# Kernel tuning notes

Hardware: AMD Instinct MI355X
Metric: run time of the kernel (lower is better)

## Reference

```python
import jax, jax.numpy as jnp
import numpy as np

N = 50000      # nodes
E = 800000     # edges (avg degree 16)
D = 3          # dim_world
L = 128        # latent_dim
STEPS = 10     # message passing steps
RID = 64       # num_rigid_ids
REMB = 16      # rigid_embedding_dim


def _mlp2(x, w1, b1, w2, b2):
    # 2-layer MLP: Linear -> ReLU -> Linear (layer_norm=False, dropout=0)
    return jnp.maximum(x @ w1 + b1, 0.0) @ w2 + b2


def setup_inputs() -> dict:
    key = jax.random.key(0)
    ks = jax.random.split(key, 24)
    f32 = jnp.float32

    def lin(k, i, o):
        return (jax.random.normal(k, (i, o), f32) / np.sqrt(i)).astype(f32)

    node_in = 2 * D + 1 + REMB   # 23
    edge_in = 2 * D + 2 + 1      # 9

    receivers = jax.random.randint(ks[4], (E,), 0, N)
    # no self edges (radius_graph uses include_self_edges=False)
    senders = (receivers + jax.random.randint(ks[3], (E,), 1, N)) % N

    inp = {
        'positions': jax.random.uniform(ks[0], (N, D), f32),
        'velocities': jax.random.normal(ks[1], (N, D), f32),
        'rigid_id': jax.random.randint(ks[2], (N,), 0, RID),
        'senders': senders,
        'receivers': receivers,
        'rigid_emb': jax.random.normal(ks[5], (RID, REMB), f32) * 0.1,
        # node encoder
        'ne_w1': lin(ks[6], node_in, L), 'ne_b1': jnp.zeros((L,), f32),
        'ne_w2': lin(ks[7], L, L),       'ne_b2': jnp.zeros((L,), f32),
        # edge encoder
        'ee_w1': lin(ks[8], edge_in, L), 'ee_b1': jnp.zeros((L,), f32),
        'ee_w2': lin(ks[9], L, L),       'ee_b2': jnp.zeros((L,), f32),
        # processor blocks (stacked over STEPS)
        'pe_w1': (jax.random.normal(ks[10], (STEPS, 3 * L, L), f32) / np.sqrt(3 * L)).astype(f32),
        'pe_b1': jnp.zeros((STEPS, L), f32),
        'pe_w2': (jax.random.normal(ks[11], (STEPS, L, L), f32) / np.sqrt(L)).astype(f32),
        'pe_b2': jnp.zeros((STEPS, L), f32),
        'pn_w1': (jax.random.normal(ks[12], (STEPS, 2 * L, L), f32) / np.sqrt(2 * L)).astype(f32),
        'pn_b1': jnp.zeros((STEPS, L), f32),
        'pn_w2': (jax.random.normal(ks[13], (STEPS, L, L), f32) / np.sqrt(L)).astype(f32),
        'pn_b2': jnp.zeros((STEPS, L), f32),
        # decoder (2 layers -> output_dim = D)
        'de_w1': lin(ks[14], L, L), 'de_b1': jnp.zeros((L,), f32),
        'de_w2': lin(ks[15], L, D), 'de_b2': jnp.zeros((D,), f32),
    }
    return inp


def reference(positions, velocities, rigid_id, senders, receivers, rigid_emb,
              ne_w1, ne_b1, ne_w2, ne_b2, ee_w1, ee_b1, ee_w2, ee_b2,
              pe_w1, pe_b1, pe_w2, pe_b2, pn_w1, pn_b1, pn_w2, pn_b2,
              de_w1, de_b1, de_w2, de_b2):
    n = positions.shape[0]
    dt = positions.dtype

    # ----- feature construction (build_gns_graph_inputs + rigid features) -----
    deg = jax.ops.segment_sum(jnp.ones(receivers.shape, dt), receivers, num_segments=n)[:, None]
    center = positions.mean(axis=0, keepdims=True)
    rigid_feat = rigid_emb[rigid_id]                                # [N, REMB]
    node_feat = jnp.concatenate([velocities, positions - center, deg, rigid_feat], axis=-1)

    rel_pos = positions[senders] - positions[receivers]             # [E, D]
    rel_vel = velocities[senders] - velocities[receivers]
    sq = jnp.sum(rel_pos * rel_pos, axis=-1, keepdims=True)
    dist = jnp.sqrt(sq)
    same = (rigid_id[senders] == rigid_id[receivers]).astype(dt)[:, None]
    edge_feat = jnp.concatenate([rel_pos, rel_vel, dist, sq, same], axis=-1)

    # ----- encode -----
    nl = _mlp2(node_feat, ne_w1, ne_b1, ne_w2, ne_b2)               # [N, L]
    el = _mlp2(edge_feat, ee_w1, ee_b1, ee_w2, ee_b2)               # [E, L]

    # ----- process: gather -> edge MLP -> scatter-add -> node MLP, residual -----
    for i in range(pe_w1.shape[0]):
        edge_in = jnp.concatenate([el, nl[senders], nl[receivers]], axis=-1)  # [E, 3L]
        el = el + _mlp2(edge_in, pe_w1[i], pe_b1[i], pe_w2[i], pe_b2[i])
        agg = jax.ops.segment_sum(el, receivers, num_segments=n)              # [N, L]
        node_in = jnp.concatenate([nl, agg], axis=-1)                         # [N, 2L]
        nl = nl + _mlp2(node_in, pn_w1[i], pn_b1[i], pn_w2[i], pn_b2[i])

    # ----- decode -----
    return _mlp2(nl, de_w1, de_b1, de_w2, de_b2)                    # [N, D]
```

## Files before the change

kernel.cpp:

```cpp
#include <hip/hip_runtime.h>
#include <hip/hip_bf16.h>

#define NN 50000
#define NE 800000
#define LDIM 128
#define NSTEPS 10

typedef __hip_bfloat16 bf16;
typedef __bf16 bf8v __attribute__((ext_vector_type(8)));
typedef float f4v __attribute__((ext_vector_type(4)));
typedef unsigned short u16x8 __attribute__((ext_vector_type(8)));

__device__ inline float bflo(unsigned int u) {
    union { unsigned int i; float f; } x; x.i = u << 16; return x.f;
}
__device__ inline float bfhi(unsigned int u) {
    union { unsigned int i; float f; } x; x.i = u & 0xffff0000u; return x.f;
}
__device__ inline unsigned short f2bf(float f) {
    __hip_bfloat16 h = __float2bfloat16(f);
    unsigned short u; __builtin_memcpy(&u, &h, 2); return u;
}


__global__ void k_hist(const int* __restrict__ rcv, int* __restrict__ cnt) {
    int i = blockIdx.x * 256 + threadIdx.x;
    if (i < NE) atomicAdd(&cnt[rcv[i]], 1);
}

__global__ __launch_bounds__(1024) void k_scan(
    const int* __restrict__ cnt, int* __restrict__ row_start,
    int* __restrict__ cur, float* __restrict__ degf) {
    __shared__ int part[1024];
    const int t = threadIdx.x;
    const int CH = (NN + 1023) / 1024;
    int b0 = t * CH, b1 = b0 + CH; if (b1 > NN) b1 = NN; if (b0 > NN) b0 = NN;
    int s = 0;
    for (int i = b0; i < b1; i++) s += cnt[i];
    part[t] = s;
    __syncthreads();
    for (int off = 1; off < 1024; off <<= 1) {
        int v = (t >= off) ? part[t - off] : 0;
        __syncthreads();
        part[t] += v;
        __syncthreads();
    }
    int run = part[t] - s;
    for (int i = b0; i < b1; i++) {
        row_start[i] = run; cur[i] = run; degf[i] = (float)cnt[i];
        run += cnt[i];
    }
    if (t == 1023) row_start[NN] = part[1023];
}

__global__ void k_scatter(const int* __restrict__ snd, const int* __restrict__ rcv,
                          int* __restrict__ cur,
                          unsigned short* __restrict__ snd_p, unsigned short* __restrict__ rcv_p) {
    int i = blockIdx.x * 256 + threadIdx.x;
    if (i < NE) {
        int r = rcv[i];
        int p = atomicAdd(&cur[r], 1);
        snd_p[p] = (unsigned short)snd[i];
        rcv_p[p] = (unsigned short)r;
    }
}

__global__ void k_center(const float* __restrict__ pos, float* __restrict__ csum) {
    __shared__ float s[3][256];
    float a = 0.f, b = 0.f, c = 0.f;
    for (int i = blockIdx.x * 256 + threadIdx.x; i < NN; i += gridDim.x * 256) {
        a += pos[3 * i]; b += pos[3 * i + 1]; c += pos[3 * i + 2];
    }
    int t = threadIdx.x;
    s[0][t] = a; s[1][t] = b; s[2][t] = c;
    __syncthreads();
    for (int off = 128; off > 0; off >>= 1) {
        if (t < off) {
            s[0][t] += s[0][t + off];
            s[1][t] += s[1][t + off];
            s[2][t] += s[2][t + off];
        }
        __syncthreads();
    }
    if (t == 0) {
        atomicAdd(&csum[0], s[0][0]);
        atomicAdd(&csum[1], s[1][0]);
        atomicAdd(&csum[2], s[2][0]);
    }
}


__global__ void k_prep_w(const float* __restrict__ w, unsigned short* __restrict__ wf,
                         int KT, int Ksrc, int lo) {
    int b = blockIdx.x;
    int s = b / (KT * 8), rem = b % (KT * 8);
    int kt = rem / 8, nt = rem % 8;
    int lane = threadIdx.x, col = lane & 15, quad = lane >> 4;
    const float* W = w + (size_t)s * Ksrc * 128;
    u16x8 o;
#pragma unroll
    for (int jj = 0; jj < 8; jj++) {
        int k = kt * 32 + quad * 8 + jj;
        float x = (k < Ksrc) ? W[(size_t)k * 128 + nt * 16 + col] : 0.f;
        unsigned short h = f2bf(x);
        if (lo) h = f2bf(x - bflo(h));
        o[jj] = h;
    }
    *(u16x8*)(wf + (((size_t)b) * 64 + lane) * 8) = o;
}


__global__ __launch_bounds__(256) void k_agg(
    const unsigned short* __restrict__ el, const int* __restrict__ row_start,
    unsigned short* __restrict__ agg) {
    const int wave = threadIdx.x >> 6, lane = threadIdx.x & 63;
    const int n = blockIdx.x * 4 + wave;
    if (n >= NN) return;
    const int sub = lane >> 4, c16 = lane & 15;
    const int st = row_start[n], en = row_start[n + 1];
    float s[8];
#pragma unroll
    for (int k = 0; k < 8; k++) s[k] = 0.f;
    for (int q = st + sub; q < en; q += 4) {
        uint4 v = *(const uint4*)(el + (size_t)q * 128 + c16 * 8);
        s[0] += bflo(v.x); s[1] += bfhi(v.x);
        s[2] += bflo(v.y); s[3] += bfhi(v.y);
        s[4] += bflo(v.z); s[5] += bfhi(v.z);
        s[6] += bflo(v.w); s[7] += bfhi(v.w);
    }
#pragma unroll
    for (int k = 0; k < 8; k++) {
        s[k] += __shfl_xor(s[k], 16);
        s[k] += __shfl_xor(s[k], 32);
    }
    if (sub == 0) {
        u16x8 o;
#pragma unroll
        for (int k = 0; k < 8; k++) o[k] = f2bf(s[k]);
        *(u16x8*)(agg + (size_t)n * 128 + c16 * 8) = o;
    }
}


__global__ __launch_bounds__(256) void k_node_enc_m(
    const float* __restrict__ pos, const float* __restrict__ vel,
    const int* __restrict__ rid, const float* __restrict__ remb,
    const float* __restrict__ degf, const float* __restrict__ csum,
    const unsigned short* __restrict__ w1h, const unsigned short* __restrict__ w1l,
    const float* __restrict__ b1,
    const unsigned short* __restrict__ w2h, const unsigned short* __restrict__ w2l,
    const float* __restrict__ b2,
    float* __restrict__ nl) {
    __shared__ __align__(16) unsigned short feat_s[32 * 72];
    __shared__ __align__(16) unsigned short hid_s[32 * 264];
    const int tid = threadIdx.x, wave = tid >> 6, lane = tid & 63;
    const int col = lane & 15, quad = lane >> 4;
    bf8v W1H[2], W1L[2], W2H[4][2], W2L[4][2];
#pragma unroll
    for (int t = 0; t < 2; t++) {
        W1H[t] = *(const bf8v*)(w1h + ((size_t)(2 * wave + t) * 64 + lane) * 8);
        W1L[t] = *(const bf8v*)(w1l + ((size_t)(2 * wave + t) * 64 + lane) * 8);
    }
#pragma unroll
    for (int kt = 0; kt < 4; kt++)
#pragma unroll
        for (int t = 0; t < 2; t++) {
            W2H[kt][t] = *(const bf8v*)(w2h + ((size_t)(kt * 8 + 2 * wave + t) * 64 + lane) * 8);
            W2L[kt][t] = *(const bf8v*)(w2l + ((size_t)(kt * 8 + 2 * wave + t) * 64 + lane) * 8);
        }
    float bias1[2], bias2[2];
#pragma unroll
    for (int t = 0; t < 2; t++) {
        bias1[t] = b1[(2 * wave + t) * 16 + col];
        bias2[t] = b2[(2 * wave + t) * 16 + col];
    }
    float cx = csum[0] * (1.0f / NN), cy = csum[1] * (1.0f / NN), cz = csum[2] * (1.0f / NN);
    uint4 z = {0u, 0u, 0u, 0u};
    for (int s2 = tid; s2 < 288; s2 += 256) *(uint4*)(feat_s + s2 * 8) = z;

    for (int it = 0; it < 4; it++) {
        const int base = blockIdx.x * 128 + it * 32;
        if (base >= NN) break;
        __syncthreads();
        if (tid < 32) {
            int n = base + tid; if (n > NN - 1) n = NN - 1;
            float v[23];
            v[0] = vel[3 * n]; v[1] = vel[3 * n + 1]; v[2] = vel[3 * n + 2];
            v[3] = pos[3 * n] - cx; v[4] = pos[3 * n + 1] - cy; v[5] = pos[3 * n + 2] - cz;
            v[6] = degf[n];
            int rb = rid[n] * 16;
#pragma unroll
            for (int k = 0; k < 16; k++) v[7 + k] = remb[rb + k];
            unsigned short* f = feat_s + tid * 72;
#pragma unroll
            for (int k = 0; k < 23; k++) {
                unsigned short h = f2bf(v[k]);
                f[k] = h; f[32 + k] = f2bf(v[k] - bflo(h));
            }
        }
        __syncthreads();
        f4v acc[2][2];
#pragma unroll
        for (int mt = 0; mt < 2; mt++)
#pragma unroll
            for (int t = 0; t < 2; t++) acc[mt][t] = (f4v){0.f, 0.f, 0.f, 0.f};
        {
            bf8v a0h = *(const bf8v*)(feat_s + col * 72 + quad * 8);
            bf8v a1h = *(const bf8v*)(feat_s + (16 + col) * 72 + quad * 8);
            bf8v a0l = *(const bf8v*)(feat_s + col * 72 + 32 + quad * 8);
            bf8v a1l = *(const bf8v*)(feat_s + (16 + col) * 72 + 32 + quad * 8);
#pragma unroll
            for (int t = 0; t < 2; t++) {
                acc[0][t] = __builtin_amdgcn_mfma_f32_16x16x32_bf16(a0h, W1H[t], acc[0][t], 0, 0, 0);
                acc[1][t] = __builtin_amdgcn_mfma_f32_16x16x32_bf16(a1h, W1H[t], acc[1][t], 0, 0, 0);
                acc[0][t] = __builtin_amdgcn_mfma_f32_16x16x32_bf16(a0l, W1H[t], acc[0][t], 0, 0, 0);
                acc[1][t] = __builtin_amdgcn_mfma_f32_16x16x32_bf16(a1l, W1H[t], acc[1][t], 0, 0, 0);
                acc[0][t] = __builtin_amdgcn_mfma_f32_16x16x32_bf16(a0h, W1L[t], acc[0][t], 0, 0, 0);
                acc[1][t] = __builtin_amdgcn_mfma_f32_16x16x32_bf16(a1h, W1L[t], acc[1][t], 0, 0, 0);
            }
        }
#pragma unroll
        for (int mt = 0; mt < 2; mt++)
#pragma unroll
            for (int t = 0; t < 2; t++) {
                const int nc = (2 * wave + t) * 16 + col;
#pragma unroll
                for (int r = 0; r < 4; r++) {
                    float h = fmaxf(acc[mt][t][r] + bias1[t], 0.f);
                    unsigned short hh = f2bf(h);
                    hid_s[(mt * 16 + quad * 4 + r) * 264 + nc] = hh;
                    hid_s[(mt * 16 + quad * 4 + r) * 264 + 128 + nc] = f2bf(h - bflo(hh));
                }
            }
        __syncthreads();
#pragma unroll
        for (int mt = 0; mt < 2; mt++)
#pragma unroll
            for (int t = 0; t < 2; t++) acc[mt][t] = (f4v){0.f, 0.f, 0.f, 0.f};
#pragma unroll
        for (int kt = 0; kt < 8; kt++) {
            int w = kt & 3;
            bf8v a0 = *(const bf8v*)(hid_s + col * 264 + kt * 32 + quad * 8);
            bf8v a1 = *(const bf8v*)(hid_s + (16 + col) * 264 + kt * 32 + quad * 8);
#pragma unroll
            for (int t = 0; t < 2; t++) {
                acc[0][t] = __builtin_amdgcn_mfma_f32_16x16x32_bf16(a0, W2H[w][t], acc[0][t], 0, 0, 0);
                acc[1][t] = __builtin_amdgcn_mfma_f32_16x16x32_bf16(a1, W2H[w][t], acc[1][t], 0, 0, 0);
            }
        }
#pragma unroll
        for (int kt = 0; kt < 4; kt++) {
            bf8v a0 = *(const bf8v*)(hid_s + col * 264 + kt * 32 + quad * 8);
            bf8v a1 = *(const bf8v*)(hid_s + (16 + col) * 264 + kt * 32 + quad * 8);
#pragma unroll
            for (int t = 0; t < 2; t++) {
                acc[0][t] = __builtin_amdgcn_mfma_f32_16x16x32_bf16(a0, W2L[kt][t], acc[0][t], 0, 0, 0);
                acc[1][t] = __builtin_amdgcn_mfma_f32_16x16x32_bf16(a1, W2L[kt][t], acc[1][t], 0, 0, 0);
            }
        }
#pragma unroll
        for (int mt = 0; mt < 2; mt++)
#pragma unroll
            for (int t = 0; t < 2; t++) {
                const int nc = (2 * wave + t) * 16 + col;
#pragma unroll
                for (int r = 0; r < 4; r++) {
                    const int row = mt * 16 + quad * 4 + r;
                    if (base + row < NN)
                        nl[(size_t)(base + row) * 128 + nc] = acc[mt][t][r] + bias2[t];
                }
            }
    }
}


__global__ __launch_bounds__(256) void k_edge_enc_m(
    const float* __restrict__ pos, const float* __restrict__ vel,
    const int* __restrict__ rid,
    const unsigned short* __restrict__ snd, const unsigned short* __restrict__ rcv,
    const unsigned short* __restrict__ w1h, const unsigned short* __restrict__ w1l,
    const float* __restrict__ b1,
    const unsigned short* __restrict__ w2h, const unsigned short* __restrict__ w2l,
    const float* __restrict__ b2,
    unsigned short* __restrict__ el) {
    __shared__ __align__(16) unsigned short feat_s[32 * 72];
    __shared__ __align__(16) unsigned short hid_s[32 * 264];
    const int tid = threadIdx.x, wave = tid >> 6, lane = tid & 63;
    const int col = lane & 15, quad = lane >> 4;
    bf8v W1H[2], W1L[2], W2H[4][2], W2L[4][2];
#pragma unroll
    for (int t = 0; t < 2; t++) {
        W1H[t] = *(const bf8v*)(w1h + ((size_t)(2 * wave + t) * 64 + lane) * 8);
        W1L[t] = *(const bf8v*)(w1l + ((size_t)(2 * wave + t) * 64 + lane) * 8);
    }
#pragma unroll
    for (int kt = 0; kt < 4; kt++)
#pragma unroll
        for (int t = 0; t < 2; t++) {
            W2H[kt][t] = *(const bf8v*)(w2h + ((size_t)(kt * 8 + 2 * wave + t) * 64 + lane) * 8);
            W2L[kt][t] = *(const bf8v*)(w2l + ((size_t)(kt * 8 + 2 * wave + t) * 64 + lane) * 8);
        }
    float bias1[2], bias2[2];
#pragma unroll
    for (int t = 0; t < 2; t++) {
        bias1[t] = b1[(2 * wave + t) * 16 + col];
        bias2[t] = b2[(2 * wave + t) * 16 + col];
    }
    uint4 z = {0u, 0u, 0u, 0u};
    for (int s2 = tid; s2 < 288; s2 += 256) *(uint4*)(feat_s + s2 * 8) = z;

    for (int it = 0; it < 4; it++) {
        const int base = blockIdx.x * 128 + it * 32;
        __syncthreads();
        if (tid < 32) {
            int e = base + tid;
            int s = snd[e], r = rcv[e];
            float v[9];
            v[0] = pos[3 * s] - pos[3 * r]; v[1] = pos[3 * s + 1] - pos[3 * r + 1]; v[2] = pos[3 * s + 2] - pos[3 * r + 2];
            v[3] = vel[3 * s] - vel[3 * r]; v[4] = vel[3 * s + 1] - vel[3 * r + 1]; v[5] = vel[3 * s + 2] - vel[3 * r + 2];
            float sq = v[0] * v[0] + v[1] * v[1] + v[2] * v[2];
            v[6] = sqrtf(sq); v[7] = sq;
            v[8] = (rid[s] == rid[r]) ? 1.f : 0.f;
            unsigned short* f = feat_s + tid * 72;
#pragma unroll
            for (int k = 0; k < 9; k++) {
                unsigned short h = f2bf(v[k]);
                f[k] = h; f[32 + k] = f2bf(v[k] - bflo(h));
            }
        }
        __syncthreads();
        f4v acc[2][2];
#pragma unroll
        for (int mt = 0; mt < 2; mt++)
#pragma unroll
            for (int t = 0; t < 2; t++) acc[mt][t] = (f4v){0.f, 0.f, 0.f, 0.f};
        {
            bf8v a0h = *(const bf8v*)(feat_s + col * 72 + quad * 8);
            bf8v a1h = *(const bf8v*)(feat_s + (16 + col) * 72 + quad * 8);
            bf8v a0l = *(const bf8v*)(feat_s + col * 72 + 32 + quad * 8);
            bf8v a1l = *(const bf8v*)(feat_s + (16 + col) * 72 + 32 + quad * 8);
#pragma unroll
            for (int t = 0; t < 2; t++) {
                acc[0][t] = __builtin_amdgcn_mfma_f32_16x16x32_bf16(a0h, W1H[t], acc[0][t], 0, 0, 0);
                acc[1][t] = __builtin_amdgcn_mfma_f32_16x16x32_bf16(a1h, W1H[t], acc[1][t], 0, 0, 0);
                acc[0][t] = __builtin_amdgcn_mfma_f32_16x16x32_bf16(a0l, W1H[t], acc[0][t], 0, 0, 0);
                acc[1][t] = __builtin_amdgcn_mfma_f32_16x16x32_bf16(a1l, W1H[t], acc[1][t], 0, 0, 0);
                acc[0][t] = __builtin_amdgcn_mfma_f32_16x16x32_bf16(a0h, W1L[t], acc[0][t], 0, 0, 0);
                acc[1][t] = __builtin_amdgcn_mfma_f32_16x16x32_bf16(a1h, W1L[t], acc[1][t], 0, 0, 0);
            }
        }
#pragma unroll
        for (int mt = 0; mt < 2; mt++)
#pragma unroll
            for (int t = 0; t < 2; t++) {
                const int nc = (2 * wave + t) * 16 + col;
#pragma unroll
                for (int r = 0; r < 4; r++) {
                    float h = fmaxf(acc[mt][t][r] + bias1[t], 0.f);
                    unsigned short hh = f2bf(h);
                    hid_s[(mt * 16 + quad * 4 + r) * 264 + nc] = hh;
                    hid_s[(mt * 16 + quad * 4 + r) * 264 + 128 + nc] = f2bf(h - bflo(hh));
                }
            }
        __syncthreads();
#pragma unroll
        for (int mt = 0; mt < 2; mt++)
#pragma unroll
            for (int t = 0; t < 2; t++) acc[mt][t] = (f4v){0.f, 0.f, 0.f, 0.f};
#pragma unroll
        for (int kt = 0; kt < 8; kt++) {
            int w = kt & 3;
            bf8v a0 = *(const bf8v*)(hid_s + col * 264 + kt * 32 + quad * 8);
            bf8v a1 = *(const bf8v*)(hid_s + (16 + col) * 264 + kt * 32 + quad * 8);
#pragma unroll
            for (int t = 0; t < 2; t++) {
                acc[0][t] = __builtin_amdgcn_mfma_f32_16x16x32_bf16(a0, W2H[w][t], acc[0][t], 0, 0, 0);
                acc[1][t] = __builtin_amdgcn_mfma_f32_16x16x32_bf16(a1, W2H[w][t], acc[1][t], 0, 0, 0);
            }
        }
#pragma unroll
        for (int kt = 0; kt < 4; kt++) {
            bf8v a0 = *(const bf8v*)(hid_s + col * 264 + kt * 32 + quad * 8);
            bf8v a1 = *(const bf8v*)(hid_s + (16 + col) * 264 + kt * 32 + quad * 8);
#pragma unroll
            for (int t = 0; t < 2; t++) {
                acc[0][t] = __builtin_amdgcn_mfma_f32_16x16x32_bf16(a0, W2L[kt][t], acc[0][t], 0, 0, 0);
                acc[1][t] = __builtin_amdgcn_mfma_f32_16x16x32_bf16(a1, W2L[kt][t], acc[1][t], 0, 0, 0);
            }
        }
        __syncthreads();
#pragma unroll
        for (int mt = 0; mt < 2; mt++)
#pragma unroll
            for (int t = 0; t < 2; t++) {
                const int nc = (2 * wave + t) * 16 + col;
#pragma unroll
                for (int r = 0; r < 4; r++)
                    hid_s[(mt * 16 + quad * 4 + r) * 264 + nc] = f2bf(acc[mt][t][r] + bias2[t]);
            }
        __syncthreads();
#pragma unroll
        for (int p = 0; p < 2; p++) {
            int s2 = p * 256 + tid, e = s2 >> 4, c16 = s2 & 15;
            *(uint4*)(el + (size_t)(base + e) * 128 + c16 * 8) =
                *(const uint4*)(hid_s + e * 264 + c16 * 8);
        }
    }
}


__global__ __launch_bounds__(256) void k_edge_step(
    unsigned short* __restrict__ el, const float* __restrict__ nl,
    const unsigned short* __restrict__ snd, const unsigned short* __restrict__ rcv,
    const unsigned short* __restrict__ w1f, const float* __restrict__ b1,
    const unsigned short* __restrict__ w2f, const float* __restrict__ b2) {
    __shared__ __align__(16) unsigned short inl_s[32 * 392];
    __shared__ __align__(16) unsigned short hid_s[32 * 136];
    __shared__ int s_idx[64];
    const int tid = threadIdx.x;
    const int wave = tid >> 6, lane = tid & 63;
    const int col = lane & 15, quad = lane >> 4;

    bf8v W1[12][2], W2[4][2];
#pragma unroll
    for (int kt = 0; kt < 12; kt++)
#pragma unroll
        for (int t = 0; t < 2; t++)
            W1[kt][t] = *(const bf8v*)(w1f + ((size_t)(kt * 8 + 2 * wave + t) * 64 + lane) * 8);
#pragma unroll
    for (int kt = 0; kt < 4; kt++)
#pragma unroll
        for (int t = 0; t < 2; t++)
            W2[kt][t] = *(const bf8v*)(w2f + ((size_t)(kt * 8 + 2 * wave + t) * 64 + lane) * 8);
    float bias1[2], bias2[2];
#pragma unroll
    for (int t = 0; t < 2; t++) {
        bias1[t] = b1[(2 * wave + t) * 16 + col];
        bias2[t] = b2[(2 * wave + t) * 16 + col];
    }

    for (int it = 0; it < 4; it++) {
        const int base = blockIdx.x * 128 + it * 32;
        if (tid < 64) s_idx[tid] = (tid < 32) ? (int)snd[base + tid] : (int)rcv[base + tid - 32];
        __syncthreads();
#pragma unroll
        for (int p = 0; p < 2; p++) {
            int s = p * 256 + tid, e = s >> 4, c16 = s & 15;
            *(uint4*)(inl_s + e * 392 + c16 * 8) =
                *(const uint4*)(el + (size_t)(base + e) * 128 + c16 * 8);
            {
                const float* src = nl + (size_t)s_idx[e] * 128 + c16 * 8;
                float4 v0 = *(const float4*)src, v1 = *(const float4*)(src + 4);
                u16x8 o;
                o[0] = f2bf(v0.x); o[1] = f2bf(v0.y); o[2] = f2bf(v0.z); o[3] = f2bf(v0.w);
                o[4] = f2bf(v1.x); o[5] = f2bf(v1.y); o[6] = f2bf(v1.z); o[7] = f2bf(v1.w);
                *(u16x8*)(inl_s + e * 392 + 128 + c16 * 8) = o;
            }
            {
                const float* src = nl + (size_t)s_idx[32 + e] * 128 + c16 * 8;
                float4 v0 = *(const float4*)src, v1 = *(const float4*)(src + 4);
                u16x8 o;
                o[0] = f2bf(v0.x); o[1] = f2bf(v0.y); o[2] = f2bf(v0.z); o[3] = f2bf(v0.w);
                o[4] = f2bf(v1.x); o[5] = f2bf(v1.y); o[6] = f2bf(v1.z); o[7] = f2bf(v1.w);
                *(u16x8*)(inl_s + e * 392 + 256 + c16 * 8) = o;
            }
        }
        __syncthreads();

        f4v acc[2][2];
#pragma unroll
        for (int mt = 0; mt < 2; mt++)
#pragma unroll
            for (int t = 0; t < 2; t++) acc[mt][t] = (f4v){0.f, 0.f, 0.f, 0.f};
#pragma unroll
        for (int kt = 0; kt < 12; kt++) {
            bf8v a0 = *(const bf8v*)(inl_s + col * 392 + kt * 32 + quad * 8);
            bf8v a1 = *(const bf8v*)(inl_s + (16 + col) * 392 + kt * 32 + quad * 8);
            acc[0][0] = __builtin_amdgcn_mfma_f32_16x16x32_bf16(a0, W1[kt][0], acc[0][0], 0, 0, 0);
            acc[0][1] = __builtin_amdgcn_mfma_f32_16x16x32_bf16(a0, W1[kt][1], acc[0][1], 0, 0, 0);
            acc[1][0] = __builtin_amdgcn_mfma_f32_16x16x32_bf16(a1, W1[kt][0], acc[1][0], 0, 0, 0);
            acc[1][1] = __builtin_amdgcn_mfma_f32_16x16x32_bf16(a1, W1[kt][1], acc[1][1], 0, 0, 0);
        }
#pragma unroll
        for (int mt = 0; mt < 2; mt++)
#pragma unroll
            for (int t = 0; t < 2; t++) {
                const int nc = (2 * wave + t) * 16 + col;
#pragma unroll
                for (int r = 0; r < 4; r++) {
                    float v = fmaxf(acc[mt][t][r] + bias1[t], 0.f);
                    hid_s[(mt * 16 + quad * 4 + r) * 136 + nc] = f2bf(v);
                }
            }
        __syncthreads();

#pragma unroll
        for (int mt = 0; mt < 2; mt++)
#pragma unroll
            for (int t = 0; t < 2; t++) acc[mt][t] = (f4v){0.f, 0.f, 0.f, 0.f};
#pragma unroll
        for (int kt = 0; kt < 4; kt++) {
            bf8v a0 = *(const bf8v*)(hid_s + col * 136 + kt * 32 + quad * 8);
            bf8v a1 = *(const bf8v*)(hid_s + (16 + col) * 136 + kt * 32 + quad * 8);
            acc[0][0] = __builtin_amdgcn_mfma_f32_16x16x32_bf16(a0, W2[kt][0], acc[0][0], 0, 0, 0);
            acc[0][1] = __builtin_amdgcn_mfma_f32_16x16x32_bf16(a0, W2[kt][1], acc[0][1], 0, 0, 0);
            acc[1][0] = __builtin_amdgcn_mfma_f32_16x16x32_bf16(a1, W2[kt][0], acc[1][0], 0, 0, 0);
            acc[1][1] = __builtin_amdgcn_mfma_f32_16x16x32_bf16(a1, W2[kt][1], acc[1][1], 0, 0, 0);
        }
        __syncthreads();
#pragma unroll
        for (int mt = 0; mt < 2; mt++)
#pragma unroll
            for (int t = 0; t < 2; t++) {
                const int nc = (2 * wave + t) * 16 + col;
#pragma unroll
                for (int r = 0; r < 4; r++) {
                    const int row = mt * 16 + quad * 4 + r;
                    float v = acc[mt][t][r] + bias2[t] + bflo((unsigned int)inl_s[row * 392 + nc]);
                    hid_s[row * 136 + nc] = f2bf(v);
                }
            }
        __syncthreads();
#pragma unroll
        for (int p = 0; p < 2; p++) {
            int s = p * 256 + tid, e = s >> 4, c16 = s & 15;
            *(uint4*)(el + (size_t)(base + e) * 128 + c16 * 8) =
                *(const uint4*)(hid_s + e * 136 + c16 * 8);
        }
    }
}


__global__ __launch_bounds__(256) void k_node_step_s(
    float* __restrict__ nl, const unsigned short* __restrict__ agg,
    const unsigned short* __restrict__ w1h, const unsigned short* __restrict__ w1l,
    const float* __restrict__ b1,
    const unsigned short* __restrict__ w2h, const unsigned short* __restrict__ w2l,
    const float* __restrict__ b2) {
    __shared__ __align__(16) unsigned short a_s[32 * 392];
    __shared__ __align__(16) unsigned short hid_s[32 * 264];
    const int tid = threadIdx.x, wave = tid >> 6, lane = tid & 63;
    const int col = lane & 15, quad = lane >> 4;
    bf8v W1H[8][2], W1L[8][2], W2H[4][2], W2L[4][2];
#pragma unroll
    for (int kt = 0; kt < 8; kt++)
#pragma unroll
        for (int t = 0; t < 2; t++) {
            W1H[kt][t] = *(const bf8v*)(w1h + ((size_t)(kt * 8 + 2 * wave + t) * 64 + lane) * 8);
            W1L[kt][t] = *(const bf8v*)(w1l + ((size_t)(kt * 8 + 2 * wave + t) * 64 + lane) * 8);
        }
#pragma unroll
    for (int kt = 0; kt < 4; kt++)
#pragma unroll
        for (int t = 0; t < 2; t++) {
            W2H[kt][t] = *(const bf8v*)(w2h + ((size_t)(kt * 8 + 2 * wave + t) * 64 + lane) * 8);
            W2L[kt][t] = *(const bf8v*)(w2l + ((size_t)(kt * 8 + 2 * wave + t) * 64 + lane) * 8);
        }
    float bias1[2], bias2[2];
#pragma unroll
    for (int t = 0; t < 2; t++) {
        bias1[t] = b1[(2 * wave + t) * 16 + col];
        bias2[t] = b2[(2 * wave + t) * 16 + col];
    }
    for (int it = 0; it < 2; it++) {
        const int base = blockIdx.x * 64 + it * 32;
        if (base >= NN) break;
        __syncthreads();
#pragma unroll
        for (int p = 0; p < 4; p++) {
            int s2 = p * 256 + tid, e = s2 >> 5, c4 = s2 & 31;
            int n = base + e; if (n > NN - 1) n = NN - 1;
            float4 v = *(const float4*)(nl + (size_t)n * 128 + c4 * 4);
            ushort4 hi, lo;
            hi.x = f2bf(v.x); lo.x = f2bf(v.x - bflo(hi.x));
            hi.y = f2bf(v.y); lo.y = f2bf(v.y - bflo(hi.y));
            hi.z = f2bf(v.z); lo.z = f2bf(v.z - bflo(hi.z));
            hi.w = f2bf(v.w); lo.w = f2bf(v.w - bflo(hi.w));
            *(ushort4*)(a_s + e * 392 + c4 * 4) = hi;
            *(ushort4*)(a_s + e * 392 + 128 + c4 * 4) = lo;
        }
#pragma unroll
        for (int p = 0; p < 2; p++) {
            int s2 = p * 256 + tid, e = s2 >> 4, c16 = s2 & 15;
            int n = base + e; if (n > NN - 1) n = NN - 1;
            *(uint4*)(a_s + e * 392 + 256 + c16 * 8) =
                *(const uint4*)(agg + (size_t)n * 128 + c16 * 8);
        }
        __syncthreads();

        f4v acc[2][2];
#pragma unroll
        for (int mt = 0; mt < 2; mt++)
#pragma unroll
            for (int t = 0; t < 2; t++) acc[mt][t] = (f4v){0.f, 0.f, 0.f, 0.f};
#pragma unroll
        for (int kt = 0; kt < 8; kt++) {
            bf8v a0 = *(const bf8v*)(a_s + col * 392 + kt * 32 + quad * 8);
            bf8v a1 = *(const bf8v*)(a_s + (16 + col) * 392 + kt * 32 + quad * 8);
#pragma unroll
            for (int t = 0; t < 2; t++) {
                acc[0][t] = __builtin_amdgcn_mfma_f32_16x16x32_bf16(a0, W1H[kt & 3][t], acc[0][t], 0, 0, 0);
                acc[1][t] = __builtin_amdgcn_mfma_f32_16x16x32_bf16(a1, W1H[kt & 3][t], acc[1][t], 0, 0, 0);
            }
        }
#pragma unroll
        for (int kt = 0; kt < 4; kt++) {
            bf8v a0 = *(const bf8v*)(a_s + col * 392 + 256 + kt * 32 + quad * 8);
            bf8v a1 = *(const bf8v*)(a_s + (16 + col) * 392 + 256 + kt * 32 + quad * 8);
#pragma unroll
            for (int t = 0; t < 2; t++) {
                acc[0][t] = __builtin_amdgcn_mfma_f32_16x16x32_bf16(a0, W1H[4 + kt][t], acc[0][t], 0, 0, 0);
                acc[1][t] = __builtin_amdgcn_mfma_f32_16x16x32_bf16(a1, W1H[4 + kt][t], acc[1][t], 0, 0, 0);
            }
        }
#pragma unroll
        for (int kt = 0; kt < 4; kt++) {
            bf8v a0 = *(const bf8v*)(a_s + col * 392 + kt * 32 + quad * 8);
            bf8v a1 = *(const bf8v*)(a_s + (16 + col) * 392 + kt * 32 + quad * 8);
#pragma unroll
            for (int t = 0; t < 2; t++) {
                acc[0][t] = __builtin_amdgcn_mfma_f32_16x16x32_bf16(a0, W1L[kt][t], acc[0][t], 0, 0, 0);
                acc[1][t] = __builtin_amdgcn_mfma_f32_16x16x32_bf16(a1, W1L[kt][t], acc[1][t], 0, 0, 0);
            }
        }
#pragma unroll
        for (int kt = 0; kt < 4; kt++) {
            bf8v a0 = *(const bf8v*)(a_s + col * 392 + 256 + kt * 32 + quad * 8);
            bf8v a1 = *(const bf8v*)(a_s + (16 + col) * 392 + 256 + kt * 32 + quad * 8);
#pragma unroll
            for (int t = 0; t < 2; t++) {
                acc[0][t] = __builtin_amdgcn_mfma_f32_16x16x32_bf16(a0, W1L[4 + kt][t], acc[0][t], 0, 0, 0);
                acc[1][t] = __builtin_amdgcn_mfma_f32_16x16x32_bf16(a1, W1L[4 + kt][t], acc[1][t], 0, 0, 0);
            }
        }
#pragma unroll
        for (int mt = 0; mt < 2; mt++)
#pragma unroll
            for (int t = 0; t < 2; t++) {
                const int nc = (2 * wave + t) * 16 + col;
#pragma unroll
                for (int r = 0; r < 4; r++) {
                    float h = fmaxf(acc[mt][t][r] + bias1[t], 0.f);
                    unsigned short hh = f2bf(h);
                    hid_s[(mt * 16 + quad * 4 + r) * 264 + nc] = hh;
                    hid_s[(mt * 16 + quad * 4 + r) * 264 + 128 + nc] = f2bf(h - bflo(hh));
                }
            }
        __syncthreads();
#pragma unroll
        for (int mt = 0; mt < 2; mt++)
#pragma unroll
            for (int t = 0; t < 2; t++) acc[mt][t] = (f4v){0.f, 0.f, 0.f, 0.f};
#pragma unroll
        for (int kt = 0; kt < 8; kt++) {
            int w = kt & 3;
            bf8v a0 = *(const bf8v*)(hid_s + col * 264 + kt * 32 + quad * 8);
            bf8v a1 = *(const bf8v*)(hid_s + (16 + col) * 264 + kt * 32 + quad * 8);
#pragma unroll
            for (int t = 0; t < 2; t++) {
                acc[0][t] = __builtin_amdgcn_mfma_f32_16x16x32_bf16(a0, W2H[w][t], acc[0][t], 0, 0, 0);
                acc[1][t] = __builtin_amdgcn_mfma_f32_16x16x32_bf16(a1, W2H[w][t], acc[1][t], 0, 0, 0);
            }
        }
#pragma unroll
        for (int kt = 0; kt < 4; kt++) {
            bf8v a0 = *(const bf8v*)(hid_s + col * 264 + kt * 32 + quad * 8);
            bf8v a1 = *(const bf8v*)(hid_s + (16 + col) * 264 + kt * 32 + quad * 8);
#pragma unroll
            for (int t = 0; t < 2; t++) {
                acc[0][t] = __builtin_amdgcn_mfma_f32_16x16x32_bf16(a0, W2L[kt][t], acc[0][t], 0, 0, 0);
                acc[1][t] = __builtin_amdgcn_mfma_f32_16x16x32_bf16(a1, W2L[kt][t], acc[1][t], 0, 0, 0);
            }
        }
#pragma unroll
        for (int mt = 0; mt < 2; mt++)
#pragma unroll
            for (int t = 0; t < 2; t++) {
                const int nc = (2 * wave + t) * 16 + col;
#pragma unroll
                for (int r = 0; r < 4; r++) {
                    const int row = mt * 16 + quad * 4 + r;
                    int n = base + row;
                    if (n < NN) {
                        float v = acc[mt][t][r] + bias2[t] + nl[(size_t)n * 128 + nc];
                        nl[(size_t)n * 128 + nc] = v;
                    }
                }
            }
    }
}


__global__ __launch_bounds__(128) void k_decode(
    const float* __restrict__ nl,
    const float* __restrict__ w1, const float* __restrict__ b1,
    const float* __restrict__ w2, const float* __restrict__ b2,
    float* __restrict__ out) {
    __shared__ float inl[16][128];
    __shared__ float hid[16][128];
    int j = threadIdx.x;
    int base = blockIdx.x * 16;
    for (int e = 0; e < 16; e++) inl[e][j] = nl[(size_t)(base + e) * 128 + j];
    __syncthreads();
    float acc[16];
#pragma unroll
    for (int e = 0; e < 16; e++) acc[e] = b1[j];
    for (int kc = 0; kc < 16; kc++) {
        float w[8];
#pragma unroll
        for (int t = 0; t < 8; t++) w[t] = w1[(kc * 8 + t) * 128 + j];
#pragma unroll
        for (int e = 0; e < 16; e++) {
            float4 h0 = *(const float4*)&inl[e][kc * 8];
            float4 h1 = *(const float4*)&inl[e][kc * 8 + 4];
            acc[e] = fmaf(h0.x, w[0], acc[e]); acc[e] = fmaf(h0.y, w[1], acc[e]);
            acc[e] = fmaf(h0.z, w[2], acc[e]); acc[e] = fmaf(h0.w, w[3], acc[e]);
            acc[e] = fmaf(h1.x, w[4], acc[e]); acc[e] = fmaf(h1.y, w[5], acc[e]);
            acc[e] = fmaf(h1.z, w[6], acc[e]); acc[e] = fmaf(h1.w, w[7], acc[e]);
        }
    }
#pragma unroll
    for (int e = 0; e < 16; e++) hid[e][j] = fmaxf(acc[e], 0.f);
    __syncthreads();
    if (j < 48) {
        int e = j / 3, ch = j - 3 * (j / 3);
        float s = b2[ch];
        for (int k = 0; k < 128; k++) s = fmaf(hid[e][k], w2[k * 3 + ch], s);
        out[(size_t)(base + e) * 3 + ch] = s;
    }
}


extern "C" void kernel_launch(void* const* d_in, const int* in_sizes, int n_in,
                              void* d_out, int out_size, void* d_ws, size_t ws_size,
                              hipStream_t stream) {
    (void)in_sizes; (void)n_in; (void)out_size; (void)ws_size;
    const float* pos   = (const float*)d_in[0];
    const float* vel   = (const float*)d_in[1];
    const int*   rid   = (const int*)d_in[2];
    const int*   snd   = (const int*)d_in[3];
    const int*   rcv   = (const int*)d_in[4];
    const float* remb  = (const float*)d_in[5];
    const float* ne_w1 = (const float*)d_in[6];
    const float* ne_b1 = (const float*)d_in[7];
    const float* ne_w2 = (const float*)d_in[8];
    const float* ne_b2 = (const float*)d_in[9];
    const float* ee_w1 = (const float*)d_in[10];
    const float* ee_b1 = (const float*)d_in[11];
    const float* ee_w2 = (const float*)d_in[12];
    const float* ee_b2 = (const float*)d_in[13];
    const float* pe_w1 = (const float*)d_in[14];
    const float* pe_b1 = (const float*)d_in[15];
    const float* pe_w2 = (const float*)d_in[16];
    const float* pe_b2 = (const float*)d_in[17];
    const float* pn_w1 = (const float*)d_in[18];
    const float* pn_b1 = (const float*)d_in[19];
    const float* pn_w2 = (const float*)d_in[20];
    const float* pn_b2 = (const float*)d_in[21];
    const float* de_w1 = (const float*)d_in[22];
    const float* de_b1 = (const float*)d_in[23];
    const float* de_w2 = (const float*)d_in[24];
    const float* de_b2 = (const float*)d_in[25];
    float* out = (float*)d_out;

    char* p = (char*)d_ws;
    auto carve = [&](size_t bytes) { void* q = (void*)p; p += (bytes + 15) & ~(size_t)15; return q; };
    unsigned short* el    = (unsigned short*)carve((size_t)NE * LDIM * 2);
    float*          nl    = (float*)carve((size_t)NN * LDIM * 4);
    unsigned short* agg   = (unsigned short*)carve((size_t)NN * LDIM * 2);
    unsigned short* w1f_e = (unsigned short*)carve((size_t)NSTEPS * 12 * 8 * 512 * 2);
    unsigned short* w2f_e = (unsigned short*)carve((size_t)NSTEPS * 4 * 8 * 512 * 2);
    unsigned short* w1h_n = (unsigned short*)carve((size_t)NSTEPS * 8 * 8 * 512 * 2);
    unsigned short* w1l_n = (unsigned short*)carve((size_t)NSTEPS * 8 * 8 * 512 * 2);
    unsigned short* w2h_n = (unsigned short*)carve((size_t)NSTEPS * 4 * 8 * 512 * 2);
    unsigned short* w2l_n = (unsigned short*)carve((size_t)NSTEPS * 4 * 8 * 512 * 2);
    unsigned short* eew1h = (unsigned short*)carve((size_t)1 * 8 * 512 * 2);
    unsigned short* eew1l = (unsigned short*)carve((size_t)1 * 8 * 512 * 2);
    unsigned short* eew2h = (unsigned short*)carve((size_t)4 * 8 * 512 * 2);
    unsigned short* eew2l = (unsigned short*)carve((size_t)4 * 8 * 512 * 2);
    unsigned short* new1h = (unsigned short*)carve((size_t)1 * 8 * 512 * 2);
    unsigned short* new1l = (unsigned short*)carve((size_t)1 * 8 * 512 * 2);
    unsigned short* new2h = (unsigned short*)carve((size_t)4 * 8 * 512 * 2);
    unsigned short* new2l = (unsigned short*)carve((size_t)4 * 8 * 512 * 2);
    unsigned short* snd_p = (unsigned short*)carve((size_t)NE * 2);
    unsigned short* rcv_p = (unsigned short*)carve((size_t)NE * 2);
    int*            rs    = (int*)carve((size_t)(NN + 1) * 4);
    int*            cnt   = (int*)carve((size_t)NN * 4);
    int*            cur   = (int*)carve((size_t)NN * 4);
    float*          degf  = (float*)carve((size_t)NN * 4);
    float*          csum  = (float*)carve(16);

    hipMemsetAsync(cnt, 0, (size_t)NN * 4, stream);
    hipMemsetAsync(csum, 0, 16, stream);
    k_hist<<<NE / 256, 256, 0, stream>>>(rcv, cnt);
    k_scan<<<1, 1024, 0, stream>>>(cnt, rs, cur, degf);
    k_center<<<64, 256, 0, stream>>>(pos, csum);
    k_scatter<<<NE / 256, 256, 0, stream>>>(snd, rcv, cur, snd_p, rcv_p);
    k_prep_w<<<NSTEPS * 12 * 8, 64, 0, stream>>>(pe_w1, w1f_e, 12, 384, 0);
    k_prep_w<<<NSTEPS * 4 * 8, 64, 0, stream>>>(pe_w2, w2f_e, 4, 128, 0);
    k_prep_w<<<NSTEPS * 8 * 8, 64, 0, stream>>>(pn_w1, w1h_n, 8, 256, 0);
    k_prep_w<<<NSTEPS * 8 * 8, 64, 0, stream>>>(pn_w1, w1l_n, 8, 256, 1);
    k_prep_w<<<NSTEPS * 4 * 8, 64, 0, stream>>>(pn_w2, w2h_n, 4, 128, 0);
    k_prep_w<<<NSTEPS * 4 * 8, 64, 0, stream>>>(pn_w2, w2l_n, 4, 128, 1);
    k_prep_w<<<8, 64, 0, stream>>>(ee_w1, eew1h, 1, 9, 0);
    k_prep_w<<<8, 64, 0, stream>>>(ee_w1, eew1l, 1, 9, 1);
    k_prep_w<<<4 * 8, 64, 0, stream>>>(ee_w2, eew2h, 4, 128, 0);
    k_prep_w<<<4 * 8, 64, 0, stream>>>(ee_w2, eew2l, 4, 128, 1);
    k_prep_w<<<8, 64, 0, stream>>>(ne_w1, new1h, 1, 23, 0);
    k_prep_w<<<8, 64, 0, stream>>>(ne_w1, new1l, 1, 23, 1);
    k_prep_w<<<4 * 8, 64, 0, stream>>>(ne_w2, new2h, 4, 128, 0);
    k_prep_w<<<4 * 8, 64, 0, stream>>>(ne_w2, new2l, 4, 128, 1);

    k_node_enc_m<<<(NN + 127) / 128, 256, 0, stream>>>(pos, vel, rid, remb, degf, csum,
                                                       new1h, new1l, ne_b1, new2h, new2l, ne_b2, nl);
    k_edge_enc_m<<<NE / 128, 256, 0, stream>>>(pos, vel, rid, snd_p, rcv_p,
                                               eew1h, eew1l, ee_b1, eew2h, eew2l, ee_b2, el);
    for (int i = 0; i < NSTEPS; i++) {
        k_edge_step<<<NE / 128, 256, 0, stream>>>(el, nl, snd_p, rcv_p,
            w1f_e + (size_t)i * 12 * 8 * 512, pe_b1 + i * 128,
            w2f_e + (size_t)i * 4 * 8 * 512, pe_b2 + i * 128);
        k_agg<<<(NN + 3) / 4, 256, 0, stream>>>(el, rs, agg);
        k_node_step_s<<<(NN + 63) / 64, 256, 0, stream>>>(nl, agg,
            w1h_n + (size_t)i * 8 * 8 * 512, w1l_n + (size_t)i * 8 * 8 * 512, pn_b1 + i * 128,
            w2h_n + (size_t)i * 4 * 8 * 512, w2l_n + (size_t)i * 4 * 8 * 512, pn_b2 + i * 128);
    }
    k_decode<<<NN / 16, 128, 0, stream>>>(nl, de_w1, de_b1, de_w2, de_b2, out);
}
```

Measured before the change: 2.944 ms.

## Store node latents as split bf16 hi/lo arrays and prefetch sender gathers

Node latents are now stored as two bf16 planes (hi and lo residual) instead of fp32. The edge step gathers only the hi plane directly with 16-byte loads and no conversion, which halves the gather bytes per sender and receiver row. Sender rows for the next sub-tile are prefetched into registers so their latency overlaps the current MFMA work. The node step reads the hi/lo planes directly and recomputes the residual from shared memory. This adds extra syncs and staging through shared memory when writing results.

```diff
diff --git a/kernel.cpp b/kernel.cpp
--- a/kernel.cpp
+++ b/kernel.cpp
@@ -150,7 +150,7 @@
     const float* __restrict__ b1,
     const unsigned short* __restrict__ w2h, const unsigned short* __restrict__ w2l,
     const float* __restrict__ b2,
-    float* __restrict__ nl) {
+    unsigned short* __restrict__ nlh, unsigned short* __restrict__ nll) {
     __shared__ __align__(16) unsigned short feat_s[32 * 72];
     __shared__ __align__(16) unsigned short hid_s[32 * 264];
     const int tid = threadIdx.x, wave = tid >> 6, lane = tid & 63;
@@ -258,6 +258,7 @@
                 acc[1][t] = __builtin_amdgcn_mfma_f32_16x16x32_bf16(a1, W2L[kt][t], acc[1][t], 0, 0, 0);
             }
         }
+        __syncthreads();
 #pragma unroll
         for (int mt = 0; mt < 2; mt++)
 #pragma unroll
@@ -266,10 +267,23 @@
 #pragma unroll
                 for (int r = 0; r < 4; r++) {
                     const int row = mt * 16 + quad * 4 + r;
-                    if (base + row < NN)
-                        nl[(size_t)(base + row) * 128 + nc] = acc[mt][t][r] + bias2[t];
+                    float v = acc[mt][t][r] + bias2[t];
+                    unsigned short hh = f2bf(v);
+                    hid_s[row * 264 + nc] = hh;
+                    hid_s[row * 264 + 128 + nc] = f2bf(v - bflo(hh));
                 }
             }
+        __syncthreads();
+#pragma unroll
+        for (int p = 0; p < 2; p++) {
+            int s2 = p * 256 + tid, e = s2 >> 4, c16 = s2 & 15;
+            if (base + e < NN) {
+                *(uint4*)(nlh + (size_t)(base + e) * 128 + c16 * 8) =
+                    *(const uint4*)(hid_s + e * 264 + c16 * 8);
+                *(uint4*)(nll + (size_t)(base + e) * 128 + c16 * 8) =
+                    *(const uint4*)(hid_s + e * 264 + 128 + c16 * 8);
+            }
+        }
     }
 }
 
@@ -410,16 +424,16 @@
 
 
 __global__ __launch_bounds__(256) void k_edge_step(
-    unsigned short* __restrict__ el, const float* __restrict__ nl,
+    unsigned short* __restrict__ el, const unsigned short* __restrict__ nlh,
     const unsigned short* __restrict__ snd, const unsigned short* __restrict__ rcv,
     const unsigned short* __restrict__ w1f, const float* __restrict__ b1,
     const unsigned short* __restrict__ w2f, const float* __restrict__ b2) {
     __shared__ __align__(16) unsigned short inl_s[32 * 392];
     __shared__ __align__(16) unsigned short hid_s[32 * 136];
-    __shared__ int s_idx[64];
     const int tid = threadIdx.x;
     const int wave = tid >> 6, lane = tid & 63;
     const int col = lane & 15, quad = lane >> 4;
+    const int erow = tid >> 4, c16 = tid & 15;
 
     bf8v W1[12][2], W2[4][2];
 #pragma unroll
@@ -439,30 +453,31 @@
         bias2[t] = b2[(2 * wave + t) * 16 + col];
     }
 
+    uint4 pf_s[2];
+#pragma unroll
+    for (int p = 0; p < 2; p++) {
+        int ge = blockIdx.x * 128 + p * 16 + erow;
+        pf_s[p] = *(const uint4*)(nlh + (size_t)snd[ge] * 128 + c16 * 8);
+    }
+
     for (int it = 0; it < 4; it++) {
         const int base = blockIdx.x * 128 + it * 32;
-        if (tid < 64) s_idx[tid] = (tid < 32) ? (int)snd[base + tid] : (int)rcv[base + tid - 32];
         __syncthreads();
 #pragma unroll
         for (int p = 0; p < 2; p++) {
-            int s = p * 256 + tid, e = s >> 4, c16 = s & 15;
+            int e = p * 16 + erow;
+            int ge = base + e;
             *(uint4*)(inl_s + e * 392 + c16 * 8) =
-                *(const uint4*)(el + (size_t)(base + e) * 128 + c16 * 8);
-            {
-                const float* src = nl + (size_t)s_idx[e] * 128 + c16 * 8;
-                float4 v0 = *(const float4*)src, v1 = *(const float4*)(src + 4);
-                u16x8 o;
-                o[0] = f2bf(v0.x); o[1] = f2bf(v0.y); o[2] = f2bf(v0.z); o[3] = f2bf(v0.w);
-                o[4] = f2bf(v1.x); o[5] = f2bf(v1.y); o[6] = f2bf(v1.z); o[7] = f2bf(v1.w);
-                *(u16x8*)(inl_s + e * 392 + 128 + c16 * 8) = o;
-            }
-            {
-                const float* src = nl + (size_t)s_idx[32 + e] * 128 + c16 * 8;
-                float4 v0 = *(const float4*)src, v1 = *(const float4*)(src + 4);
-                u16x8 o;
-                o[0] = f2bf(v0.x); o[1] = f2bf(v0.y); o[2] = f2bf(v0.z); o[3] = f2bf(v0.w);
-                o[4] = f2bf(v1.x); o[5] = f2bf(v1.y); o[6] = f2bf(v1.z); o[7] = f2bf(v1.w);
-                *(u16x8*)(inl_s + e * 392 + 256 + c16 * 8) = o;
+                *(const uint4*)(el + (size_t)ge * 128 + c16 * 8);
+            *(uint4*)(inl_s + e * 392 + 128 + c16 * 8) = pf_s[p];
+            *(uint4*)(inl_s + e * 392 + 256 + c16 * 8) =
+                *(const uint4*)(nlh + (size_t)rcv[ge] * 128 + c16 * 8);
+        }
+        if (it < 3) {
+#pragma unroll
+            for (int p = 0; p < 2; p++) {
+                int ge = base + 32 + p * 16 + erow;
+                pf_s[p] = *(const uint4*)(nlh + (size_t)snd[ge] * 128 + c16 * 8);
             }
         }
         __syncthreads();
@@ -523,7 +538,7 @@
         __syncthreads();
 #pragma unroll
         for (int p = 0; p < 2; p++) {
-            int s = p * 256 + tid, e = s >> 4, c16 = s & 15;
+            int e = p * 16 + erow;
             *(uint4*)(el + (size_t)(base + e) * 128 + c16 * 8) =
                 *(const uint4*)(hid_s + e * 136 + c16 * 8);
         }
@@ -532,7 +547,8 @@
 
 
 __global__ __launch_bounds__(256) void k_node_step_s(
-    float* __restrict__ nl, const unsigned short* __restrict__ agg,
+    unsigned short* __restrict__ nlh, unsigned short* __restrict__ nll,
+    const unsigned short* __restrict__ agg,
     const unsigned short* __restrict__ w1h, const unsigned short* __restrict__ w1l,
     const float* __restrict__ b1,
     const unsigned short* __restrict__ w2h, const unsigned short* __restrict__ w2l,
@@ -567,22 +583,13 @@
         if (base >= NN) break;
         __syncthreads();
 #pragma unroll
-        for (int p = 0; p < 4; p++) {
-            int s2 = p * 256 + tid, e = s2 >> 5, c4 = s2 & 31;
+        for (int p = 0; p < 2; p++) {
+            int e = p * 16 + (tid >> 4), c16 = tid & 15;
             int n = base + e; if (n > NN - 1) n = NN - 1;
-            float4 v = *(const float4*)(nl + (size_t)n * 128 + c4 * 4);
-            ushort4 hi, lo;
-            hi.x = f2bf(v.x); lo.x = f2bf(v.x - bflo(hi.x));
-            hi.y = f2bf(v.y); lo.y = f2bf(v.y - bflo(hi.y));
-            hi.z = f2bf(v.z); lo.z = f2bf(v.z - bflo(hi.z));
-            hi.w = f2bf(v.w); lo.w = f2bf(v.w - bflo(hi.w));
-            *(ushort4*)(a_s + e * 392 + c4 * 4) = hi;
-            *(ushort4*)(a_s + e * 392 + 128 + c4 * 4) = lo;
-        }
-#pragma unroll
-        for (int p = 0; p < 2; p++) {
-            int s2 = p * 256 + tid, e = s2 >> 4, c16 = s2 & 15;
-            int n = base + e; if (n > NN - 1) n = NN - 1;
+            *(uint4*)(a_s + e * 392 + c16 * 8) =
+                *(const uint4*)(nlh + (size_t)n * 128 + c16 * 8);
+            *(uint4*)(a_s + e * 392 + 128 + c16 * 8) =
+                *(const uint4*)(nll + (size_t)n * 128 + c16 * 8);
             *(uint4*)(a_s + e * 392 + 256 + c16 * 8) =
                 *(const uint4*)(agg + (size_t)n * 128 + c16 * 8);
         }
@@ -672,6 +679,7 @@
                 acc[1][t] = __builtin_amdgcn_mfma_f32_16x16x32_bf16(a1, W2L[kt][t], acc[1][t], 0, 0, 0);
             }
         }
+        __syncthreads();
 #pragma unroll
         for (int mt = 0; mt < 2; mt++)
 #pragma unroll
@@ -680,19 +688,31 @@
 #pragma unroll
                 for (int r = 0; r < 4; r++) {
                     const int row = mt * 16 + quad * 4 + r;
-                    int n = base + row;
-                    if (n < NN) {
-                        float v = acc[mt][t][r] + bias2[t] + nl[(size_t)n * 128 + nc];
-                        nl[(size_t)n * 128 + nc] = v;
-                    }
+                    float res = bflo((unsigned int)a_s[row * 392 + nc]) +
+                                bflo((unsigned int)a_s[row * 392 + 128 + nc]);
+                    float v = acc[mt][t][r] + bias2[t] + res;
+                    unsigned short hh = f2bf(v);
+                    hid_s[row * 264 + nc] = hh;
+                    hid_s[row * 264 + 128 + nc] = f2bf(v - bflo(hh));
                 }
             }
+        __syncthreads();
+#pragma unroll
+        for (int p = 0; p < 2; p++) {
+            int e = p * 16 + (tid >> 4), c16 = tid & 15;
+            if (base + e < NN) {
+                *(uint4*)(nlh + (size_t)(base + e) * 128 + c16 * 8) =
+                    *(const uint4*)(hid_s + e * 264 + c16 * 8);
+                *(uint4*)(nll + (size_t)(base + e) * 128 + c16 * 8) =
+                    *(const uint4*)(hid_s + e * 264 + 128 + c16 * 8);
+            }
+        }
     }
 }
 
 
 __global__ __launch_bounds__(128) void k_decode(
-    const float* __restrict__ nl,
+    const unsigned short* __restrict__ nlh, const unsigned short* __restrict__ nll,
     const float* __restrict__ w1, const float* __restrict__ b1,
     const float* __restrict__ w2, const float* __restrict__ b2,
     float* __restrict__ out) {
@@ -700,7 +720,9 @@
     __shared__ float hid[16][128];
     int j = threadIdx.x;
     int base = blockIdx.x * 16;
-    for (int e = 0; e < 16; e++) inl[e][j] = nl[(size_t)(base + e) * 128 + j];
+    for (int e = 0; e < 16; e++)
+        inl[e][j] = bflo((unsigned int)nlh[(size_t)(base + e) * 128 + j]) +
+                    bflo((unsigned int)nll[(size_t)(base + e) * 128 + j]);
     __syncthreads();
     float acc[16];
 #pragma unroll
@@ -766,7 +788,8 @@
     char* p = (char*)d_ws;
     auto carve = [&](size_t bytes) { void* q = (void*)p; p += (bytes + 15) & ~(size_t)15; return q; };
     unsigned short* el    = (unsigned short*)carve((size_t)NE * LDIM * 2);
-    float*          nl    = (float*)carve((size_t)NN * LDIM * 4);
+    unsigned short* nlh   = (unsigned short*)carve((size_t)NN * LDIM * 2);
+    unsigned short* nll   = (unsigned short*)carve((size_t)NN * LDIM * 2);
     unsigned short* agg   = (unsigned short*)carve((size_t)NN * LDIM * 2);
     unsigned short* w1f_e = (unsigned short*)carve((size_t)NSTEPS * 12 * 8 * 512 * 2);
     unsigned short* w2f_e = (unsigned short*)carve((size_t)NSTEPS * 4 * 8 * 512 * 2);
@@ -812,17 +835,17 @@
     k_prep_w<<<4 * 8, 64, 0, stream>>>(ne_w2, new2l, 4, 128, 1);
 
     k_node_enc_m<<<(NN + 127) / 128, 256, 0, stream>>>(pos, vel, rid, remb, degf, csum,
-                                                       new1h, new1l, ne_b1, new2h, new2l, ne_b2, nl);
+                                                       new1h, new1l, ne_b1, new2h, new2l, ne_b2, nlh, nll);
     k_edge_enc_m<<<NE / 128, 256, 0, stream>>>(pos, vel, rid, snd_p, rcv_p,
                                                eew1h, eew1l, ee_b1, eew2h, eew2l, ee_b2, el);
     for (int i = 0; i < NSTEPS; i++) {
-        k_edge_step<<<NE / 128, 256, 0, stream>>>(el, nl, snd_p, rcv_p,
+        k_edge_step<<<NE / 128, 256, 0, stream>>>(el, nlh, snd_p, rcv_p,
             w1f_e + (size_t)i * 12 * 8 * 512, pe_b1 + i * 128,
             w2f_e + (size_t)i * 4 * 8 * 512, pe_b2 + i * 128);
         k_agg<<<(NN + 3) / 4, 256, 0, stream>>>(el, rs, agg);
-        k_node_step_s<<<(NN + 63) / 64, 256, 0, stream>>>(nl, agg,
+        k_node_step_s<<<(NN + 63) / 64, 256, 0, stream>>>(nlh, nll, agg,
             w1h_n + (size_t)i * 8 * 8 * 512, w1l_n + (size_t)i * 8 * 8 * 512, pn_b1 + i * 128,
             w2h_n + (size_t)i * 4 * 8 * 512, w2l_n + (size_t)i * 4 * 8 * 512, pn_b2 + i * 128);
     }
-    k_decode<<<NN / 16, 128, 0, stream>>>(nl, de_w1, de_b1, de_w2, de_b2, out);
-}
+    k_decode<<<NN / 16, 128, 0, stream>>>(nlh, nll, de_w1, de_b1, de_w2, de_b2, out);
+}
```

Measured after the change: 2.915 ms. No clear change (-1.0%).
